# Kernel tuning notes

Hardware: AMD Instinct MI355X
Metric: run time of the kernel (lower is better)

Reference implementation:

```python
import jax, jax.numpy as jnp
import numpy as np

T = 2048       # tokens (flattened, single causal sequence)
HID = 2048     # hidden_size
H = 16         # num_heads
DN = 128       # qk_nope_head_dim
DR = 64        # qk_rope_head_dim
DV = 128       # v_head_dim
DQK = DN + DR  # 192
QLR = 1536     # q_lora_rank
KVLR = 512     # kv_lora_rank
THETA = 10000.0
EPS = 1e-6
SCALE = DQK ** -0.5


def rmsnorm(x, w):
    return x * jax.lax.rsqrt(jnp.mean(x * x, axis=-1, keepdims=True) + EPS) * w


def rope_interleaved(x, cos, sin):
    # is_neox_style=False: rotate interleaved even/odd pairs
    x1 = x[..., 0::2]
    x2 = x[..., 1::2]
    out = jnp.stack([x1 * cos - x2 * sin, x2 * cos + x1 * sin], axis=-1)
    return out.reshape(x.shape)


def setup_inputs() -> dict:
    key = jax.random.key(0)
    ks = jax.random.split(key, 8)
    s = 0.02
    return {
        "positions": jnp.arange(T, dtype=jnp.int32),
        "hidden_states": jax.random.normal(ks[0], (T, HID), jnp.float32),
        "w_q_a": jax.random.normal(ks[1], (HID, QLR), jnp.float32) * s,
        "q_a_ln_w": jnp.ones((QLR,), jnp.float32),
        "w_q_b": jax.random.normal(ks[2], (QLR, H * DQK), jnp.float32) * s,
        "w_kv_a": jax.random.normal(ks[3], (HID, KVLR + DR), jnp.float32) * s,
        "kv_a_ln_w": jnp.ones((KVLR,), jnp.float32),
        "w_kv_b": jax.random.normal(ks[4], (KVLR, H * (DN + DV)), jnp.float32) * s,
        "w_o": jax.random.normal(ks[5], (H * DV, HID), jnp.float32) * s,
    }


def reference(positions, hidden_states, w_q_a, q_a_ln_w, w_q_b, w_kv_a,
              kv_a_ln_w, w_kv_b, w_o):
    t = hidden_states.shape[0]
    # --- Q low-rank path ---
    q = rmsnorm(hidden_states @ w_q_a, q_a_ln_w) @ w_q_b          # [T, H*DQK]
    q = q.reshape(t, H, DQK)
    q_nope, q_pe = q[..., :DN], q[..., DN:]
    # --- KV latent path ---
    latent = hidden_states @ w_kv_a                                # [T, KVLR+DR]
    kv_a = rmsnorm(latent[:, :KVLR], kv_a_ln_w)
    kv = (kv_a @ w_kv_b).reshape(t, H, DN + DV)
    k_nope, v = kv[..., :DN], kv[..., DN:]
    k_pe = latent[:, None, KVLR:]                                  # [T, 1, DR]
    # --- partial RoPE (non-neox, interleaved) ---
    inv_freq = 1.0 / (THETA ** (jnp.arange(0, DR, 2, dtype=jnp.float32) / DR))
    ang = positions.astype(jnp.float32)[:, None] * inv_freq        # [T, DR/2]
    cos = jnp.cos(ang)[:, None, :]
    sin = jnp.sin(ang)[:, None, :]
    q_pe = rope_interleaved(q_pe, cos, sin)
    k_pe = rope_interleaved(k_pe, cos, sin)
    q = jnp.concatenate([q_nope, q_pe], axis=-1)                   # [T, H, DQK]
    k = jnp.concatenate([k_nope, jnp.broadcast_to(k_pe, (t, H, DR))], axis=-1)
    # --- causal attention (V zero-padded to DQK then sliced == using V directly) ---
    scores = jnp.einsum("thd,shd->hts", q, k) * SCALE              # [H, T, T]
    causal = positions[None, :, None] >= positions[None, None, :]
    scores = jnp.where(causal, scores, jnp.finfo(scores.dtype).min)
    probs = jax.nn.softmax(scores, axis=-1)
    attn = jnp.einsum("hts,shd->thd", probs, v)                    # [T, H, DV]
    return attn.reshape(t, H * DV) @ w_o                           # [T, HID]
```

## Files before the change

kernel.cpp:

```cpp
#include <hip/hip_runtime.h>
#include <hip/hip_bf16.h>

#define T_ 2048
#define SCALE_ 0.07216878364870322f

typedef __bf16 bf16x8 __attribute__((ext_vector_type(8)));
typedef float f32x4 __attribute__((ext_vector_type(4)));
typedef float f32x16 __attribute__((ext_vector_type(16)));

__device__ inline bf16x8 load8f(const float* p) {
    const float4* f = reinterpret_cast<const float4*>(p);
    float4 a = f[0], b = f[1];
    bf16x8 r;
    r[0] = (__bf16)a.x; r[1] = (__bf16)a.y; r[2] = (__bf16)a.z; r[3] = (__bf16)a.w;
    r[4] = (__bf16)b.x; r[5] = (__bf16)b.y; r[6] = (__bf16)b.z; r[7] = (__bf16)b.w;
    return r;
}

__device__ inline void gld_lds16(const void* g, void* l) {
    __builtin_amdgcn_global_load_lds((const __attribute__((address_space(1))) void*)g,
                                     (__attribute__((address_space(3))) void*)l, 16, 0, 0);
}

__global__ __launch_bounds__(256) void cvt_bf16(const float* __restrict__ in,
                                                __bf16* __restrict__ out, int n8)
{
    int i = blockIdx.x * 256 + threadIdx.x;
    if (i < n8)
        *reinterpret_cast<bf16x8*>(out + (size_t)i * 8) = load8f(in + (size_t)i * 8);
}

__global__ __launch_bounds__(256) void transpose_cvt(
    const float* __restrict__ W, __bf16* __restrict__ Wt, int K, int N)
{
    __shared__ __bf16 tl[64][72];
    const int k0 = blockIdx.x * 64, n0 = blockIdx.y * 64;
    const int tid = threadIdx.x;
    const bool in = n0 < N;
    #pragma unroll
    for (int it = 0; it < 2; ++it) {
        int chunk = tid + it * 256;
        int r = chunk >> 3;
        int c8 = (chunk & 7) * 8;
        float4 a = {0,0,0,0}, b = {0,0,0,0};
        if (in) {
            const float* p = W + (size_t)(k0 + r) * N + n0 + c8;
            a = *reinterpret_cast<const float4*>(p);
            b = *reinterpret_cast<const float4*>(p + 4);
        }
        tl[c8+0][r] = (__bf16)a.x; tl[c8+1][r] = (__bf16)a.y;
        tl[c8+2][r] = (__bf16)a.z; tl[c8+3][r] = (__bf16)a.w;
        tl[c8+4][r] = (__bf16)b.x; tl[c8+5][r] = (__bf16)b.y;
        tl[c8+6][r] = (__bf16)b.z; tl[c8+7][r] = (__bf16)b.w;
    }
    __syncthreads();
    #pragma unroll
    for (int it = 0; it < 2; ++it) {
        int chunk = tid + it * 256;
        int n = chunk >> 3;
        int k8 = (chunk & 7) * 8;
        bf16x8 v = *reinterpret_cast<const bf16x8*>(&tl[n][k8]);
        *reinterpret_cast<bf16x8*>(Wt + (size_t)(n0 + n) * K + k0 + k8) = v;
    }
}

template <typename TC>
__global__ __launch_bounds__(256) void gemm_bt(
    const __bf16* __restrict__ A, const __bf16* __restrict__ Bt,
    TC* __restrict__ C, int M, int N, int K, int Nstore, int ldc)
{
    __shared__ __bf16 As[2][128 * 64];
    __shared__ __bf16 Bs[2][128 * 64];
    const int tid = threadIdx.x, lane = tid & 63, wid = tid >> 6;
    const int l15 = lane & 15, lg = lane >> 4;
    const int m0 = blockIdx.x * 128, n0 = blockIdx.y * 128;
    const int wr = (wid >> 1) * 64, wc = (wid & 1) * 64;

    const int srow = wid * 32 + (lane >> 3);
    const int scol = ((lane & 7) ^ (lane >> 3)) * 8;
    const __bf16* Ag = A  + (size_t)(m0 + srow) * K + scol;
    const __bf16* Bg = Bt + (size_t)(n0 + srow) * K + scol;
    const int lbase = wid * 4096;

    f32x4 acc[4][4] = {};

    {
        char* la = (char*)&As[0][0] + lbase;
        char* lb = (char*)&Bs[0][0] + lbase;
        #pragma unroll
        for (int i = 0; i < 4; ++i) {
            gld_lds16(Ag + (size_t)i * 8 * K, la + i * 1024);
            gld_lds16(Bg + (size_t)i * 8 * K, lb + i * 1024);
        }
    }
    __syncthreads();

    int cur = 0;
    for (int k0 = 0; k0 < K; k0 += 64) {
        if (k0 + 64 < K) {
            char* la = (char*)&As[cur ^ 1][0] + lbase;
            char* lb = (char*)&Bs[cur ^ 1][0] + lbase;
            #pragma unroll
            for (int i = 0; i < 4; ++i) {
                gld_lds16(Ag + (size_t)i * 8 * K + k0 + 64, la + i * 1024);
                gld_lds16(Bg + (size_t)i * 8 * K + k0 + 64, lb + i * 1024);
            }
        }

        bf16x8 af[4][2], bf[4][2];
        #pragma unroll
        for (int i = 0; i < 4; ++i) {
            const int Ra = wr + i * 16 + l15;
            const int Rb = wc + i * 16 + l15;
            const int ca = (lg ^ (Ra & 7)) * 16;
            const int cb = (lg ^ (Rb & 7)) * 16;
            const char* pa = (const char*)&As[cur][0] + Ra * 128;
            const char* pb = (const char*)&Bs[cur][0] + Rb * 128;
            af[i][0] = *reinterpret_cast<const bf16x8*>(pa + ca);
            af[i][1] = *reinterpret_cast<const bf16x8*>(pa + (ca ^ 64));
            bf[i][0] = *reinterpret_cast<const bf16x8*>(pb + cb);
            bf[i][1] = *reinterpret_cast<const bf16x8*>(pb + (cb ^ 64));
        }
        #pragma unroll
        for (int h = 0; h < 2; ++h)
            #pragma unroll
            for (int i = 0; i < 4; ++i)
                #pragma unroll
                for (int j = 0; j < 4; ++j)
                    acc[i][j] = __builtin_amdgcn_mfma_f32_16x16x32_bf16(af[i][h], bf[j][h], acc[i][j], 0, 0, 0);

        __syncthreads();
        cur ^= 1;
    }

    #pragma unroll
    for (int i = 0; i < 4; ++i)
        #pragma unroll
        for (int j = 0; j < 4; ++j)
            #pragma unroll
            for (int e = 0; e < 4; ++e) {
                int r = m0 + wr + i * 16 + lg * 4 + e;
                int c = n0 + wc + j * 16 + l15;
                if (c < Nstore)
                    C[(size_t)r * ldc + c] = (TC)acc[i][j][e];
            }
}

__global__ __launch_bounds__(256) void rmsnorm_k(
    const __bf16* __restrict__ in, int in_stride,
    const float* __restrict__ w,
    __bf16* __restrict__ out, int out_stride, int W)
{
    const int t = blockIdx.x, tid = threadIdx.x;
    const __bf16* row = in + (size_t)t * in_stride;
    float x[8];
    float ss = 0.f;
    const bool act = tid * 8 < W;
    if (act) {
        bf16x8 v = *reinterpret_cast<const bf16x8*>(row + tid * 8);
        #pragma unroll
        for (int e = 0; e < 8; ++e) { x[e] = (float)v[e]; ss += x[e] * x[e]; }
    }
    #pragma unroll
    for (int m = 1; m < 64; m <<= 1) ss += __shfl_xor(ss, m, 64);
    __shared__ float red[4];
    if ((tid & 63) == 0) red[tid >> 6] = ss;
    __syncthreads();
    float tot = red[0] + red[1] + red[2] + red[3];
    float scale = rsqrtf(tot / (float)W + 1e-6f);
    if (act) {
        float4 w0 = *reinterpret_cast<const float4*>(w + tid * 8);
        float4 w1 = *reinterpret_cast<const float4*>(w + tid * 8 + 4);
        bf16x8 o;
        o[0] = (__bf16)(x[0] * scale * w0.x); o[1] = (__bf16)(x[1] * scale * w0.y);
        o[2] = (__bf16)(x[2] * scale * w0.z); o[3] = (__bf16)(x[3] * scale * w0.w);
        o[4] = (__bf16)(x[4] * scale * w1.x); o[5] = (__bf16)(x[5] * scale * w1.y);
        o[6] = (__bf16)(x[6] * scale * w1.z); o[7] = (__bf16)(x[7] * scale * w1.w);
        *reinterpret_cast<bf16x8*>(out + (size_t)t * out_stride + tid * 8) = o;
    }
}

__global__ __launch_bounds__(256) void rope_q(
    const int* __restrict__ positions, __bf16* __restrict__ q)
{
    const int t = blockIdx.x, tid = threadIdx.x;
    __shared__ float cs[32], sn[32];
    if (tid < 32) {
        float pos = (float)positions[t];
        float invf = powf(10000.f, -(float)tid / 32.f);
        cs[tid] = cosf(pos * invf); sn[tid] = sinf(pos * invf);
    }
    __syncthreads();
    #pragma unroll
    for (int it = 0; it < 2; ++it) {
        int p = tid + it * 256;
        int h = p >> 5, i = p & 31;
        size_t base = (size_t)t * 3072 + h * 192 + 128 + 2 * i;
        float x1 = (float)q[base], x2 = (float)q[base + 1];
        q[base]     = (__bf16)(x1 * cs[i] - x2 * sn[i]);
        q[base + 1] = (__bf16)(x2 * cs[i] + x1 * sn[i]);
    }
}

__global__ __launch_bounds__(256) void kprep(
    const int* __restrict__ positions, const __bf16* __restrict__ kv,
    const __bf16* __restrict__ qkv_a, __bf16* __restrict__ kh)
{
    const int t = blockIdx.x, tid = threadIdx.x;
    __shared__ __bf16 kpe[64];
    if (tid < 32) {
        float pos = (float)positions[t];
        float invf = powf(10000.f, -(float)tid / 32.f);
        float c = cosf(pos * invf), s = sinf(pos * invf);
        float x1 = (float)qkv_a[(size_t)t * 2176 + 2048 + 2 * tid];
        float x2 = (float)qkv_a[(size_t)t * 2176 + 2049 + 2 * tid];
        kpe[2 * tid]     = (__bf16)(x1 * c - x2 * s);
        kpe[2 * tid + 1] = (__bf16)(x2 * c + x1 * s);
    }
    __syncthreads();
    const int h = tid >> 4, c = tid & 15;
    bf16x8 v = *reinterpret_cast<const bf16x8*>(kv + (size_t)t * 4096 + h * 256 + c * 8);
    *reinterpret_cast<bf16x8*>(kh + ((size_t)h * T_ + t) * 192 + c * 8) = v;
    if (c < 8) {
        bf16x8 p = *reinterpret_cast<const bf16x8*>(&kpe[c * 8]);
        *reinterpret_cast<bf16x8*>(kh + ((size_t)h * T_ + t) * 192 + 128 + c * 8) = p;
    }
}

__global__ __launch_bounds__(256) void vtrans(
    const __bf16* __restrict__ kv, __bf16* __restrict__ vt)
{
    __shared__ __bf16 tile[128][72];
    const int t0 = blockIdx.x * 64;
    const int h  = blockIdx.y;
    const int tid = threadIdx.x;
    #pragma unroll
    for (int it = 0; it < 4; ++it) {
        int chunk = tid + it * 256;
        int r = chunk >> 4;
        int d8 = (chunk & 15) * 8;
        bf16x8 v = *reinterpret_cast<const bf16x8*>(kv + (size_t)(t0 + r) * 4096 + h * 256 + 128 + d8);
        #pragma unroll
        for (int e = 0; e < 8; ++e) tile[d8 + e][r] = v[e];
    }
    __syncthreads();
    #pragma unroll
    for (int it = 0; it < 4; ++it) {
        int chunk = tid + it * 256;
        int d = chunk >> 3;
        int t8 = (chunk & 7) * 8;
        bf16x8 v = *reinterpret_cast<const bf16x8*>(&tile[d][t8]);
        *reinterpret_cast<bf16x8*>(vt + ((size_t)h * 128 + d) * 2048 + t0 + t8) = v;
    }
}

__device__ inline unsigned pk2(float a, float b) {
    union { __bf16 h[2]; unsigned u; } z;
    z.h[0] = (__bf16)a; z.h[1] = (__bf16)b;
    return z.u;
}

__global__ __launch_bounds__(512, 2) void attn_flash(
    const __bf16* __restrict__ q, const __bf16* __restrict__ kh,
    const __bf16* __restrict__ vt, __bf16* __restrict__ attn)
{
    const int tid = threadIdx.x;
    const int lane = tid & 63, wid = tid >> 6;
    const int q31 = lane & 31, hi = lane >> 5;
    const int b = blockIdx.x;
    const int h = b & 15, x = b >> 4;
    const int g = wid >> 2;
    const int par = wid & 3;
    const int myqt = g ? (63 - x) : x;
    const int q0 = myqt * 32;

    __shared__ float mls[2][8][32];
    __shared__ float linv_s[2][32];
    __shared__ float obuf[2][32][129];

    const __bf16* Kh = kh + (size_t)h * T_ * 192;
    const __bf16* Vt = vt + (size_t)h * 128 * T_;
    const __bf16* Qp = q + (size_t)(q0 + q31) * 3072 + h * 192;

    bf16x8 aq[12];
    #pragma unroll
    for (int c = 0; c < 12; ++c)
        aq[c] = *reinterpret_cast<const bf16x8*>(Qp + c * 16 + hi * 8);

    f32x16 o[4] = {};
    float m_i = -1e30f, l_i = 0.f;
    const int ntile = myqt + 1;

    bf16x8 kc[12];
    if (par < ntile) {
        const __bf16* Kp = Kh + (size_t)(par * 32 + q31) * 192 + hi * 8;
        #pragma unroll
        for (int c = 0; c < 12; ++c)
            kc[c] = *reinterpret_cast<const bf16x8*>(Kp + c * 16);
    }

    for (int it = par; it < ntile; it += 4) {
        const int s0 = it * 32;
        const bool notlast = (it + 4 < ntile);
        const __bf16* Kpn = Kh + (size_t)((it + 4) * 32 + q31) * 192 + hi * 8;

        bf16x8 vf[4][2];
        #pragma unroll
        for (int n = 0; n < 4; ++n)
            #pragma unroll
            for (int m = 0; m < 2; ++m)
                vf[n][m] = *reinterpret_cast<const bf16x8*>(
                    Vt + (size_t)(n * 32 + q31) * 2048 + s0 + (2 * m + hi) * 8);

        f32x16 sA = {}, sB = {};
        __builtin_amdgcn_s_setprio(1);
        #pragma unroll
        for (int c = 0; c < 12; c += 2) {
            sA = __builtin_amdgcn_mfma_f32_32x32x16_bf16(kc[c],     aq[c],     sA, 0, 0, 0);
            sB = __builtin_amdgcn_mfma_f32_32x32x16_bf16(kc[c + 1], aq[c + 1], sB, 0, 0, 0);
        }
        __builtin_amdgcn_s_setprio(0);

        bf16x8 kn[8];
        if (notlast) {
            #pragma unroll
            for (int c = 0; c < 8; ++c)
                kn[c] = *reinterpret_cast<const bf16x8*>(Kpn + c * 16);
        }

        float v[16];
        #pragma unroll
        for (int r = 0; r < 16; ++r) v[r] = (sA[r] + sB[r]) * SCALE_;
        if (it == myqt) {
            #pragma unroll
            for (int r = 0; r < 16; ++r) {
                int crow = (r & 3) + 8 * (r >> 2) + 4 * hi;
                if (crow > q31) v[r] = -1e30f;
            }
        }
        float mx = v[0];
        #pragma unroll
        for (int r = 1; r < 16; ++r) mx = fmaxf(mx, v[r]);
        mx = fmaxf(mx, __shfl_xor(mx, 32, 64));
        const bool skip = __all(mx <= m_i);
        float mnew = fmaxf(m_i, mx);
        float fsc = skip ? 1.f : __expf(m_i - mnew);
        m_i = mnew;
        float ps = 0.f;
        #pragma unroll
        for (int r = 0; r < 16; ++r) { v[r] = __expf(v[r] - mnew); ps += v[r]; }
        ps += __shfl_xor(ps, 32, 64);
        l_i = l_i * fsc + ps;
        if (!skip) {
            #pragma unroll
            for (int n = 0; n < 4; ++n) o[n] *= fsc;
        }

        unsigned w[8], xw[8];
        #pragma unroll
        for (int i = 0; i < 8; ++i) w[i] = pk2(v[2 * i], v[2 * i + 1]);
        #pragma unroll
        for (int i = 0; i < 8; ++i) xw[i] = __shfl_xor(w[i], 32, 64);
        union { unsigned u[4]; bf16x8 v; } P0, P1;
        P0.u[0] = hi ? xw[2] : w[0]; P0.u[1] = hi ? xw[3] : w[1];
        P0.u[2] = hi ? w[2] : xw[0]; P0.u[3] = hi ? w[3] : xw[1];
        P1.u[0] = hi ? xw[6] : w[4]; P1.u[1] = hi ? xw[7] : w[5];
        P1.u[2] = hi ? w[6] : xw[4]; P1.u[3] = hi ? w[7] : xw[5];

        __builtin_amdgcn_s_setprio(1);
        #pragma unroll
        for (int n = 0; n < 4; ++n) {
            o[n] = __builtin_amdgcn_mfma_f32_32x32x16_bf16(vf[n][0], P0.v, o[n], 0, 0, 0);
            o[n] = __builtin_amdgcn_mfma_f32_32x32x16_bf16(vf[n][1], P1.v, o[n], 0, 0, 0);
        }
        __builtin_amdgcn_s_setprio(0);

        if (notlast) {
            #pragma unroll
            for (int c = 0; c < 8; ++c) kc[c] = kn[c];
            #pragma unroll
            for (int c = 8; c < 12; ++c)
                kc[c] = *reinterpret_cast<const bf16x8*>(Kpn + c * 16);
        }
    }

    if (hi == 0) { mls[0][wid][q31] = m_i; mls[1][wid][q31] = l_i; }
    __syncthreads();
    const int gb = g * 4;
    float M = fmaxf(fmaxf(mls[0][gb][q31], mls[0][gb + 1][q31]),
                    fmaxf(mls[0][gb + 2][q31], mls[0][gb + 3][q31]));
    float L = mls[1][gb][q31]     * __expf(mls[0][gb][q31] - M)
            + mls[1][gb + 1][q31] * __expf(mls[0][gb + 1][q31] - M)
            + mls[1][gb + 2][q31] * __expf(mls[0][gb + 2][q31] - M)
            + mls[1][gb + 3][q31] * __expf(mls[0][gb + 3][q31] - M);
    float F = __expf(m_i - M);
    if (par == 0 && hi == 0) linv_s[g][q31] = 1.f / L;

    #pragma unroll
    for (int rd = 0; rd < 4; ++rd) {
        if (par == rd) {
            if (rd == 0) {
                #pragma unroll
                for (int n = 0; n < 4; ++n)
                    #pragma unroll
                    for (int r = 0; r < 16; ++r) {
                        int d = (r & 3) + 8 * (r >> 2) + 4 * hi + 32 * n;
                        obuf[g][q31][d] = F * o[n][r];
                    }
            } else {
                #pragma unroll
                for (int n = 0; n < 4; ++n)
                    #pragma unroll
                    for (int r = 0; r < 16; ++r) {
                        int d = (r & 3) + 8 * (r >> 2) + 4 * hi + 32 * n;
                        obuf[g][q31][d] += F * o[n][r];
                    }
            }
        }
        __syncthreads();
    }

    const int gtid = tid & 255;
    #pragma unroll
    for (int it = 0; it < 2; ++it) {
        int c = gtid + it * 256;
        int row = c >> 4, c8 = (c & 15) * 8;
        float inv = linv_s[g][row];
        bf16x8 vv;
        #pragma unroll
        for (int j = 0; j < 8; ++j)
            vv[j] = (__bf16)(obuf[g][row][c8 + j] * inv);
        *reinterpret_cast<bf16x8*>(attn + (size_t)(q0 + row) * 2048 + h * 128 + c8) = vv;
    }
}

extern "C" void kernel_launch(void* const* d_in, const int* in_sizes, int n_in,
                              void* d_out, int out_size, void* d_ws, size_t ws_size,
                              hipStream_t stream)
{
    const int*   positions = (const int*)d_in[0];
    const float* hidden    = (const float*)d_in[1];
    const float* w_q_a     = (const float*)d_in[2];
    const float* q_a_ln_w  = (const float*)d_in[3];
    const float* w_q_b     = (const float*)d_in[4];
    const float* w_kv_a    = (const float*)d_in[5];
    const float* kv_a_ln_w = (const float*)d_in[6];
    const float* w_kv_b    = (const float*)d_in[7];
    const float* w_o       = (const float*)d_in[8];

    char* ws = (char*)d_ws;
    __bf16* hidden_bf = (__bf16*)(ws);
    __bf16* vt        = (__bf16*)(ws);
    __bf16* wbuf      = (__bf16*)(ws + 8388608);
    __bf16* qkv_a     = (__bf16*)(ws + 17825792);
    __bf16* attn      = (__bf16*)(ws + 17825792);
    __bf16* q_a_n     = (__bf16*)(ws + 26738688);
    __bf16* q         = (__bf16*)(ws + 33030144);
    __bf16* kv_a_n    = (__bf16*)(ws + 45613056);
    __bf16* kv        = (__bf16*)(ws + 47710208);
    __bf16* kh        = (__bf16*)(ws + 64487424);

    dim3 blk(256);
    cvt_bf16<<<dim3(2048), blk, 0, stream>>>(hidden, hidden_bf, 524288);

    transpose_cvt<<<dim3(32, 24), blk, 0, stream>>>(w_q_a, wbuf, 2048, 1536);
    transpose_cvt<<<dim3(32, 10), blk, 0, stream>>>(w_kv_a, wbuf + (size_t)1536 * 2048, 2048, 576);
    gemm_bt<__bf16><<<dim3(16, 17), blk, 0, stream>>>(hidden_bf, wbuf, qkv_a, 2048, 2176, 2048, 2112, 2176);
    rmsnorm_k<<<dim3(2048), blk, 0, stream>>>(qkv_a, 2176, q_a_ln_w, q_a_n, 1536, 1536);
    rmsnorm_k<<<dim3(2048), blk, 0, stream>>>(qkv_a + 1536, 2176, kv_a_ln_w, kv_a_n, 512, 512);

    transpose_cvt<<<dim3(24, 48), blk, 0, stream>>>(w_q_b, wbuf, 1536, 3072);
    gemm_bt<__bf16><<<dim3(16, 24), blk, 0, stream>>>(q_a_n, wbuf, q, 2048, 3072, 1536, 3072, 3072);

    transpose_cvt<<<dim3(8, 64), blk, 0, stream>>>(w_kv_b, wbuf, 512, 4096);
    gemm_bt<__bf16><<<dim3(16, 32), blk, 0, stream>>>(kv_a_n, wbuf, kv, 2048, 4096, 512, 4096, 4096);

    rope_q<<<dim3(2048), blk, 0, stream>>>(positions, q);
    kprep<<<dim3(2048), blk, 0, stream>>>(positions, kv, qkv_a, kh);
    vtrans<<<dim3(32, 16), blk, 0, stream>>>(kv, vt);
    attn_flash<<<dim3(512), dim3(512), 0, stream>>>(q, kh, vt, attn);

    transpose_cvt<<<dim3(32, 32), blk, 0, stream>>>(w_o, wbuf, 2048, 2048);
    gemm_bt<float><<<dim3(16, 16), blk, 0, stream>>>(attn, wbuf, (float*)d_out, 2048, 2048, 2048, 2048, 2048);
}
```

Measured before the change: 258.9 us.

## Fuse small kernels and batch Q/KV up-projection GEMMs into one launch

```diff
diff --git a/kernel.cpp b/kernel.cpp
--- a/kernel.cpp
+++ b/kernel.cpp
@@ -65,15 +65,13 @@
 }
 
 template <typename TC>
-__global__ __launch_bounds__(256) void gemm_bt(
+__device__ __forceinline__ void gemm_body(
     const __bf16* __restrict__ A, const __bf16* __restrict__ Bt,
-    TC* __restrict__ C, int M, int N, int K, int Nstore, int ldc)
-{
-    __shared__ __bf16 As[2][128 * 64];
-    __shared__ __bf16 Bs[2][128 * 64];
+    TC* __restrict__ C, int K, int Nstore, int ldc, int m0, int n0,
+    __bf16* As, __bf16* Bs)
+{
     const int tid = threadIdx.x, lane = tid & 63, wid = tid >> 6;
     const int l15 = lane & 15, lg = lane >> 4;
-    const int m0 = blockIdx.x * 128, n0 = blockIdx.y * 128;
     const int wr = (wid >> 1) * 64, wc = (wid & 1) * 64;
 
     const int srow = wid * 32 + (lane >> 3);
@@ -85,8 +83,8 @@
     f32x4 acc[4][4] = {};
 
     {
-        char* la = (char*)&As[0][0] + lbase;
-        char* lb = (char*)&Bs[0][0] + lbase;
+        char* la = (char*)As + lbase;
+        char* lb = (char*)Bs + lbase;
         #pragma unroll
         for (int i = 0; i < 4; ++i) {
             gld_lds16(Ag + (size_t)i * 8 * K, la + i * 1024);
@@ -98,8 +96,8 @@
     int cur = 0;
     for (int k0 = 0; k0 < K; k0 += 64) {
         if (k0 + 64 < K) {
-            char* la = (char*)&As[cur ^ 1][0] + lbase;
-            char* lb = (char*)&Bs[cur ^ 1][0] + lbase;
+            char* la = (char*)As + (cur ^ 1) * 16384 + lbase;
+            char* lb = (char*)Bs + (cur ^ 1) * 16384 + lbase;
             #pragma unroll
             for (int i = 0; i < 4; ++i) {
                 gld_lds16(Ag + (size_t)i * 8 * K + k0 + 64, la + i * 1024);
@@ -114,8 +112,8 @@
             const int Rb = wc + i * 16 + l15;
             const int ca = (lg ^ (Ra & 7)) * 16;
             const int cb = (lg ^ (Rb & 7)) * 16;
-            const char* pa = (const char*)&As[cur][0] + Ra * 128;
-            const char* pb = (const char*)&Bs[cur][0] + Rb * 128;
+            const char* pa = (const char*)As + cur * 16384 + Ra * 128;
+            const char* pb = (const char*)Bs + cur * 16384 + Rb * 128;
             af[i][0] = *reinterpret_cast<const bf16x8*>(pa + ca);
             af[i][1] = *reinterpret_cast<const bf16x8*>(pa + (ca ^ 64));
             bf[i][0] = *reinterpret_cast<const bf16x8*>(pb + cb);
@@ -146,49 +144,87 @@
             }
 }
 
-__global__ __launch_bounds__(256) void rmsnorm_k(
-    const __bf16* __restrict__ in, int in_stride,
-    const float* __restrict__ w,
-    __bf16* __restrict__ out, int out_stride, int W)
-{
-    const int t = blockIdx.x, tid = threadIdx.x;
-    const __bf16* row = in + (size_t)t * in_stride;
+template <typename TC>
+__global__ __launch_bounds__(256) void gemm_bt(
+    const __bf16* __restrict__ A, const __bf16* __restrict__ Bt,
+    TC* __restrict__ C, int M, int N, int K, int Nstore, int ldc)
+{
+    __shared__ __bf16 As[2 * 128 * 64];
+    __shared__ __bf16 Bs[2 * 128 * 64];
+    gemm_body<TC>(A, Bt, C, K, Nstore, ldc, blockIdx.x * 128, blockIdx.y * 128, As, Bs);
+}
+
+__global__ __launch_bounds__(256) void gemm_bt_pair(
+    const __bf16* __restrict__ A0, const __bf16* __restrict__ B0, __bf16* __restrict__ C0,
+    int N0, int K0, int nby0,
+    const __bf16* __restrict__ A1, const __bf16* __restrict__ B1, __bf16* __restrict__ C1,
+    int N1, int K1)
+{
+    __shared__ __bf16 As[2 * 128 * 64];
+    __shared__ __bf16 Bs[2 * 128 * 64];
+    if ((int)blockIdx.y < nby0)
+        gemm_body<__bf16>(A0, B0, C0, K0, N0, N0, blockIdx.x * 128, blockIdx.y * 128, As, Bs);
+    else
+        gemm_body<__bf16>(A1, B1, C1, K1, N1, N1, blockIdx.x * 128, (blockIdx.y - nby0) * 128, As, Bs);
+}
+
+__global__ __launch_bounds__(256) void rmsnorm_fused(
+    const __bf16* __restrict__ qkv_a,
+    const float* __restrict__ qw, const float* __restrict__ kw,
+    __bf16* __restrict__ q_a_n, __bf16* __restrict__ kv_a_n)
+{
+    const int t = blockIdx.x, tid = threadIdx.x, wid = tid >> 6;
+    const bool isq = tid < 192;
+    const __bf16* src = qkv_a + (size_t)t * 2176 + (isq ? tid * 8 : 1536 + (tid - 192) * 8);
     float x[8];
     float ss = 0.f;
-    const bool act = tid * 8 < W;
-    if (act) {
-        bf16x8 v = *reinterpret_cast<const bf16x8*>(row + tid * 8);
-        #pragma unroll
-        for (int e = 0; e < 8; ++e) { x[e] = (float)v[e]; ss += x[e] * x[e]; }
-    }
+    bf16x8 v = *reinterpret_cast<const bf16x8*>(src);
+    #pragma unroll
+    for (int e = 0; e < 8; ++e) { x[e] = (float)v[e]; ss += x[e] * x[e]; }
     #pragma unroll
     for (int m = 1; m < 64; m <<= 1) ss += __shfl_xor(ss, m, 64);
     __shared__ float red[4];
-    if ((tid & 63) == 0) red[tid >> 6] = ss;
+    if ((tid & 63) == 0) red[wid] = ss;
     __syncthreads();
-    float tot = red[0] + red[1] + red[2] + red[3];
-    float scale = rsqrtf(tot / (float)W + 1e-6f);
-    if (act) {
-        float4 w0 = *reinterpret_cast<const float4*>(w + tid * 8);
-        float4 w1 = *reinterpret_cast<const float4*>(w + tid * 8 + 4);
-        bf16x8 o;
-        o[0] = (__bf16)(x[0] * scale * w0.x); o[1] = (__bf16)(x[1] * scale * w0.y);
-        o[2] = (__bf16)(x[2] * scale * w0.z); o[3] = (__bf16)(x[3] * scale * w0.w);
-        o[4] = (__bf16)(x[4] * scale * w1.x); o[5] = (__bf16)(x[5] * scale * w1.y);
-        o[6] = (__bf16)(x[6] * scale * w1.z); o[7] = (__bf16)(x[7] * scale * w1.w);
-        *reinterpret_cast<bf16x8*>(out + (size_t)t * out_stride + tid * 8) = o;
-    }
-}
-
-__global__ __launch_bounds__(256) void rope_q(
-    const int* __restrict__ positions, __bf16* __restrict__ q)
+    float scale;
+    const float* w;
+    if (isq) {
+        scale = rsqrtf((red[0] + red[1] + red[2]) / 1536.f + 1e-6f);
+        w = qw + tid * 8;
+    } else {
+        scale = rsqrtf(red[3] / 512.f + 1e-6f);
+        w = kw + (tid - 192) * 8;
+    }
+    float4 w0 = *reinterpret_cast<const float4*>(w);
+    float4 w1 = *reinterpret_cast<const float4*>(w + 4);
+    bf16x8 o;
+    o[0] = (__bf16)(x[0] * scale * w0.x); o[1] = (__bf16)(x[1] * scale * w0.y);
+    o[2] = (__bf16)(x[2] * scale * w0.z); o[3] = (__bf16)(x[3] * scale * w0.w);
+    o[4] = (__bf16)(x[4] * scale * w1.x); o[5] = (__bf16)(x[5] * scale * w1.y);
+    o[6] = (__bf16)(x[6] * scale * w1.z); o[7] = (__bf16)(x[7] * scale * w1.w);
+    if (isq)
+        *reinterpret_cast<bf16x8*>(q_a_n + (size_t)t * 1536 + tid * 8) = o;
+    else
+        *reinterpret_cast<bf16x8*>(kv_a_n + (size_t)t * 512 + (tid - 192) * 8) = o;
+}
+
+__global__ __launch_bounds__(256) void rope_kprep(
+    const int* __restrict__ positions, __bf16* __restrict__ q,
+    const __bf16* __restrict__ kv, const __bf16* __restrict__ qkv_a,
+    __bf16* __restrict__ kh)
 {
     const int t = blockIdx.x, tid = threadIdx.x;
     __shared__ float cs[32], sn[32];
+    __shared__ __bf16 kpe[64];
     if (tid < 32) {
         float pos = (float)positions[t];
         float invf = powf(10000.f, -(float)tid / 32.f);
-        cs[tid] = cosf(pos * invf); sn[tid] = sinf(pos * invf);
+        float c = cosf(pos * invf), s = sinf(pos * invf);
+        cs[tid] = c; sn[tid] = s;
+        float x1 = (float)qkv_a[(size_t)t * 2176 + 2048 + 2 * tid];
+        float x2 = (float)qkv_a[(size_t)t * 2176 + 2049 + 2 * tid];
+        kpe[2 * tid]     = (__bf16)(x1 * c - x2 * s);
+        kpe[2 * tid + 1] = (__bf16)(x2 * c + x1 * s);
     }
     __syncthreads();
     #pragma unroll
@@ -200,24 +236,6 @@
         q[base]     = (__bf16)(x1 * cs[i] - x2 * sn[i]);
         q[base + 1] = (__bf16)(x2 * cs[i] + x1 * sn[i]);
     }
-}
-
-__global__ __launch_bounds__(256) void kprep(
-    const int* __restrict__ positions, const __bf16* __restrict__ kv,
-    const __bf16* __restrict__ qkv_a, __bf16* __restrict__ kh)
-{
-    const int t = blockIdx.x, tid = threadIdx.x;
-    __shared__ __bf16 kpe[64];
-    if (tid < 32) {
-        float pos = (float)positions[t];
-        float invf = powf(10000.f, -(float)tid / 32.f);
-        float c = cosf(pos * invf), s = sinf(pos * invf);
-        float x1 = (float)qkv_a[(size_t)t * 2176 + 2048 + 2 * tid];
-        float x2 = (float)qkv_a[(size_t)t * 2176 + 2049 + 2 * tid];
-        kpe[2 * tid]     = (__bf16)(x1 * c - x2 * s);
-        kpe[2 * tid + 1] = (__bf16)(x2 * c + x1 * s);
-    }
-    __syncthreads();
     const int h = tid >> 4, c = tid & 15;
     bf16x8 v = *reinterpret_cast<const bf16x8*>(kv + (size_t)t * 4096 + h * 256 + c * 8);
     *reinterpret_cast<bf16x8*>(kh + ((size_t)h * T_ + t) * 192 + c * 8) = v;
@@ -321,11 +339,14 @@
         }
         __builtin_amdgcn_s_setprio(0);
 
-        bf16x8 kn[8];
+        bf16x8 kn[12];
         if (notlast) {
             #pragma unroll
-            for (int c = 0; c < 8; ++c)
+            for (int c = 0; c < 12; ++c) {
                 kn[c] = *reinterpret_cast<const bf16x8*>(Kpn + c * 16);
+                unsigned* kw_ = reinterpret_cast<unsigned*>(&kn[c]);
+                asm volatile("" : "+v"(kw_[0]), "+v"(kw_[1]), "+v"(kw_[2]), "+v"(kw_[3]));
+            }
         }
 
         float v[16];
@@ -377,10 +398,7 @@
 
         if (notlast) {
             #pragma unroll
-            for (int c = 0; c < 8; ++c) kc[c] = kn[c];
-            #pragma unroll
-            for (int c = 8; c < 12; ++c)
-                kc[c] = *reinterpret_cast<const bf16x8*>(Kpn + c * 16);
+            for (int c = 0; c < 12; ++c) kc[c] = kn[c];
         }
     }
 
@@ -459,6 +477,7 @@
     __bf16* kv_a_n    = (__bf16*)(ws + 45613056);
     __bf16* kv        = (__bf16*)(ws + 47710208);
     __bf16* kh        = (__bf16*)(ws + 64487424);
+    __bf16* wbuf2     = (__bf16*)(ws + 77070336);
 
     dim3 blk(256);
     cvt_bf16<<<dim3(2048), blk, 0, stream>>>(hidden, hidden_bf, 524288);
@@ -466,17 +485,15 @@
     transpose_cvt<<<dim3(32, 24), blk, 0, stream>>>(w_q_a, wbuf, 2048, 1536);
     transpose_cvt<<<dim3(32, 10), blk, 0, stream>>>(w_kv_a, wbuf + (size_t)1536 * 2048, 2048, 576);
     gemm_bt<__bf16><<<dim3(16, 17), blk, 0, stream>>>(hidden_bf, wbuf, qkv_a, 2048, 2176, 2048, 2112, 2176);
-    rmsnorm_k<<<dim3(2048), blk, 0, stream>>>(qkv_a, 2176, q_a_ln_w, q_a_n, 1536, 1536);
-    rmsnorm_k<<<dim3(2048), blk, 0, stream>>>(qkv_a + 1536, 2176, kv_a_ln_w, kv_a_n, 512, 512);
+    rmsnorm_fused<<<dim3(2048), blk, 0, stream>>>(qkv_a, q_a_ln_w, kv_a_ln_w, q_a_n, kv_a_n);
 
     transpose_cvt<<<dim3(24, 48), blk, 0, stream>>>(w_q_b, wbuf, 1536, 3072);
-    gemm_bt<__bf16><<<dim3(16, 24), blk, 0, stream>>>(q_a_n, wbuf, q, 2048, 3072, 1536, 3072, 3072);
-
-    transpose_cvt<<<dim3(8, 64), blk, 0, stream>>>(w_kv_b, wbuf, 512, 4096);
-    gemm_bt<__bf16><<<dim3(16, 32), blk, 0, stream>>>(kv_a_n, wbuf, kv, 2048, 4096, 512, 4096, 4096);
-
-    rope_q<<<dim3(2048), blk, 0, stream>>>(positions, q);
-    kprep<<<dim3(2048), blk, 0, stream>>>(positions, kv, qkv_a, kh);
+    transpose_cvt<<<dim3(8, 64), blk, 0, stream>>>(w_kv_b, wbuf2, 512, 4096);
+    gemm_bt_pair<<<dim3(16, 56), blk, 0, stream>>>(
+        q_a_n, wbuf, q, 3072, 1536, 24,
+        kv_a_n, wbuf2, kv, 4096, 512);
+
+    rope_kprep<<<dim3(2048), blk, 0, stream>>>(positions, q, kv, qkv_a, kh);
     vtrans<<<dim3(32, 16), blk, 0, stream>>>(kv, vt);
     attn_flash<<<dim3(512), dim3(512), 0, stream>>>(q, kh, vt, attn);
 
```

Result: slower. 301.4 us (+16.4%).
